# Performance work log

Hardware: AMD Instinct MI355X
Metric: run time of the kernel (lower is better)

Reference implementation:

```python
import jax, jax.numpy as jnp
import numpy as np

Z, K, H, Y = 128, 256, 512, 4  # z_size, key_size, hidden_size, y_dim


def setup_inputs() -> dict:
    key = jax.random.key(0)
    ks = jax.random.split(key, 8)
    B, T, P = 512, 32, 32
    s = lambda k, shape, sc: (jax.random.normal(k, shape, jnp.float32) * sc)
    return {
        "x_seq": jax.random.normal(ks[0], (B, T, P, P), jnp.float32),
        "W_enc": s(ks[1], (P * P, Z), 0.03),
        "gamma": jnp.ones((Z,), jnp.float32),
        "beta": jnp.zeros((Z,), jnp.float32),
        "W_ih": s(ks[2], (4 * H, K + 1), 0.05),
        "W_hh": s(ks[3], (4 * H, H), 0.04),
        "b_ih": jnp.zeros((4 * H,), jnp.float32),
        "b_hh": jnp.zeros((4 * H,), jnp.float32),
        "W_key": s(ks[4], (K, H), 0.06),
        "b_key": jnp.zeros((K,), jnp.float32),
        "W_g": s(ks[5], (1, H), 0.06),
        "b_g": jnp.zeros((1,), jnp.float32),
        "conf_gain": jnp.ones((1,), jnp.float32),
        "conf_bias": jnp.zeros((1,), jnp.float32),
        "W_y": s(ks[6], (Y, H), 0.06),
        "b_y": jnp.zeros((Y,), jnp.float32),
    }


def _lstm_cell(x, h, c, W_ih, W_hh, b_ih, b_hh):
    # PyTorch gate order: i, f, g, o
    gates = x @ W_ih.T + b_ih + h @ W_hh.T + b_hh
    i, f, g, o = jnp.split(gates, 4, axis=-1)
    c = jax.nn.sigmoid(f) * c + jax.nn.sigmoid(i) * jnp.tanh(g)
    h = jax.nn.sigmoid(o) * jnp.tanh(c)
    return h, c


def _forward(x_seq, W_enc, gamma, beta, W_ih, W_hh, b_ih, b_hh,
             W_key, b_key, W_g, b_g, conf_gain, conf_bias, W_y, b_y):
    B, T, P, _ = x_seq.shape
    # encoder: flatten -> linear to z_size (stand-in for Encoder_mlp)
    z = x_seq.reshape(B, T, P * P) @ W_enc  # [B, T, Z]
    # context norm over the sequence dim (single task segment)
    mu = z.mean(axis=1, keepdims=True)
    sig = jnp.sqrt(z.var(axis=1, keepdims=True) + 1e-8)
    z = (z - mu) / sig * gamma + beta

    M = T + 1  # T+1 steps; final step feeds a zero z_t
    z_pad = jnp.concatenate([z, jnp.zeros((B, 1, Z), z.dtype)], axis=1)  # [B, M, Z]

    h0 = jnp.zeros((B, H), z.dtype)
    c0 = jnp.zeros((B, H), z.dtype)
    kr0 = jnp.zeros((B, K + 1), z.dtype)
    Mk0 = jnp.zeros((B, M, K), z.dtype)
    Mv0 = jnp.zeros((B, M, Z), z.dtype)

    def step(carry, t):
        h, c, key_r, M_k, M_v = carry
        z_t = jax.lax.dynamic_index_in_dim(z_pad, t, axis=1, keepdims=False)  # [B, Z]
        h, c = _lstm_cell(key_r, h, c, W_ih, W_hh, b_ih, b_hh)
        key_w = jax.nn.relu(h @ W_key.T + b_key)          # [B, K]
        g = jax.nn.sigmoid(h @ W_g.T + b_g)               # [B, 1]
        y_lin = h @ W_y.T + b_y                            # [B, Y]
        # attention read over valid memory slots j < t
        scores = jnp.einsum('bz,bmz->bm', z_t, M_v)        # [B, M]
        valid = (jnp.arange(M) < t)[None, :]
        w_k = jax.nn.softmax(jnp.where(valid, scores, -1e9), axis=1)
        c_k = jax.nn.sigmoid(scores * conf_gain + conf_bias)
        kv = jnp.concatenate([M_k, c_k[..., None]], axis=2)  # [B, M, K+1]
        attn = g * jnp.einsum('bm,bmd->bd', w_k, kv)          # [B, K+1]
        key_r_new = jnp.where(t == 0, jnp.zeros_like(attn), attn)
        # append to memory at slot t
        M_k = jax.lax.dynamic_update_slice_in_dim(M_k, key_w[:, None, :], t, axis=1)
        M_v = jax.lax.dynamic_update_slice_in_dim(M_v, z_t[:, None, :], t, axis=1)
        return (h, c, key_r_new, M_k, M_v), y_lin

    _, ys = jax.lax.scan(step, (h0, c0, kr0, Mk0, Mv0), jnp.arange(M))
    return ys[-1]  # y_pred_linear from final step, [B, Y]


def reference(x_seq, W_enc, gamma, beta, W_ih, W_hh, b_ih, b_hh,
              W_key, b_key, W_g, b_g, conf_gain, conf_bias, W_y, b_y):
    y_pred_linear = _forward(x_seq, W_enc, gamma, beta, W_ih, W_hh, b_ih, b_hh,
                             W_key, b_key, W_g, b_g, conf_gain, conf_bias, W_y, b_y)
    y_pred = jnp.argmax(y_pred_linear, axis=1)
    return y_pred_linear, y_pred
```

## Files before the change

### kernel.cpp

```cpp
#include <hip/hip_runtime.h>
#include <math.h>

typedef unsigned short ushort;
typedef unsigned int uint;
typedef __bf16 bf16x8 __attribute__((ext_vector_type(8)));
typedef float f32x4 __attribute__((ext_vector_type(4)));

#define ZS    128
#define KS    256
#define HS    512
#define BATCH 512
#define TT    32
#define MM    33
#define NB    2304
#define KPAD  800
#define HOFF  272
#define LDA   800

static __device__ __forceinline__ float sigf(float x) { return 1.f / (1.f + expf(-x)); }
static __device__ __forceinline__ float bf2f(ushort u) { return __uint_as_float((uint)u << 16); }

__global__ void prep_w(const float* __restrict__ W_ih, const float* __restrict__ W_hh,
                       const float* __restrict__ W_key, const float* __restrict__ b_ih,
                       const float* __restrict__ b_hh, const float* __restrict__ b_key,
                       const float* __restrict__ W_enc,
                       ushort* __restrict__ Whi, ushort* __restrict__ Wlo,
                       ushort* __restrict__ Behi, ushort* __restrict__ Belo,
                       float* __restrict__ biasN)
{
    int idx = blockIdx.x * 256 + threadIdx.x;
    if (idx < NB) {
        float bv;
        if (idx < 2048) { int j = idx >> 2, gi = idx & 3, r = gi * 512 + j; bv = b_ih[r] + b_hh[r]; }
        else bv = b_key[idx - 2048];
        biasN[idx] = bv;
    }
    if (idx < NB * KPAD) {
        int n = idx / KPAD, k = idx - n * KPAD;
        float v = 0.f;
        if (n < 2048) {
            int j = n >> 2, gi = n & 3, r = gi * 512 + j;
            if (k < 257) v = W_ih[r * 257 + k];
            else if (k >= HOFF && k < HOFF + 512) v = W_hh[r * 512 + (k - HOFF)];
        } else {
            if (k >= HOFF && k < HOFF + 512) v = W_key[(n - 2048) * 512 + (k - HOFF)];
        }
        uint u = __float_as_uint(v);
        Whi[idx] = (ushort)(u >> 16);
        float lo = v - __uint_as_float(u & 0xFFFF0000u);
        Wlo[idx] = (ushort)(__float_as_uint(lo) >> 16);
    } else if (idx < NB * KPAD + 128 * 1024) {
        int e = idx - NB * KPAD;
        int n = e >> 10, k = e & 1023;
        float v = W_enc[k * 128 + n];
        uint u = __float_as_uint(v);
        Behi[e] = (ushort)(u >> 16);
        float lo = v - __uint_as_float(u & 0xFFFF0000u);
        Belo[e] = (ushort)(__float_as_uint(lo) >> 16);
    }
}

template<int BN, int MODE, bool PRESPLIT>
__global__ __launch_bounds__(256, 4)
void gemm_mfma(const float* __restrict__ A,
               const ushort* __restrict__ Ahi, const ushort* __restrict__ Alo, int lda,
               const ushort* __restrict__ Bhi, const ushort* __restrict__ Blo, int ldb,
               int nslice,
               float* __restrict__ out,
               ushort* __restrict__ outHi, ushort* __restrict__ outLo,
               const float* __restrict__ biasN,
               float* __restrict__ cst, float* __restrict__ Mk, int step)
{
    constexpr int NI = BN / 32;
    constexpr int AHI = 0, ALO = 32 * 40, BHI = 64 * 40, BLO = 64 * 40 + BN * 40;
    constexpr int BUF = 64 * 40 + 2 * BN * 40;
    __shared__ ushort lds[2 * BUF];

    const int tid = threadIdx.x;
    const int bx = blockIdx.x, by = blockIdx.y;
    const int row0 = by * 32, n0 = bx * BN;
    const int l = tid & 63, w = tid >> 6, wm = w >> 1, wn = w & 1;
    const int lm = l & 15, kg = (l >> 4) << 3;

    f32x4 acc[NI];
    const f32x4 zero4 = {0.f, 0.f, 0.f, 0.f};
#pragma unroll
    for (int ni = 0; ni < NI; ni++) acc[ni] = zero4;

    float4 avf;
    uint4 avu;
    uint4 bhv[BN / 64], blv[BN / 64];

    auto LOADG = [&](int s) {
        const int k0 = s * 32;
        if (PRESPLIT) {
            int idx = tid & 127, r = idx >> 2, c = (idx & 3) << 3;
            const ushort* src = (tid < 128) ? Ahi : Alo;
            avu = *(const uint4*)(src + (size_t)(row0 + r) * lda + k0 + c);
        } else {
            int r = tid >> 3, c = (tid & 7) << 2;
            avf = *(const float4*)(A + (size_t)(row0 + r) * lda + k0 + c);
        }
#pragma unroll
        for (int i = 0; i < BN / 64; i++) {
            int idx = tid + 256 * i, r = idx >> 2, c = (idx & 3) << 3;
            bhv[i] = *(const uint4*)(Bhi + (size_t)(n0 + r) * ldb + k0 + c);
            blv[i] = *(const uint4*)(Blo + (size_t)(n0 + r) * ldb + k0 + c);
        }
    };
    auto STORE = [&](int buf) {
        ushort* L = lds + buf * BUF;
        if (PRESPLIT) {
            int idx = tid & 127, r = idx >> 2, c = (idx & 3) << 3;
            *(uint4*)&L[(tid < 128 ? AHI : ALO) + r * 40 + c] = avu;
        } else {
            int r = tid >> 3, c = (tid & 7) << 2;
            uint u0 = __float_as_uint(avf.x), u1 = __float_as_uint(avf.y);
            uint u2 = __float_as_uint(avf.z), u3 = __float_as_uint(avf.w);
            uint hp0 = (u1 & 0xFFFF0000u) | (u0 >> 16);
            uint hp1 = (u3 & 0xFFFF0000u) | (u2 >> 16);
            float l0 = avf.x - __uint_as_float(u0 & 0xFFFF0000u);
            float l1 = avf.y - __uint_as_float(u1 & 0xFFFF0000u);
            float l2 = avf.z - __uint_as_float(u2 & 0xFFFF0000u);
            float l3 = avf.w - __uint_as_float(u3 & 0xFFFF0000u);
            uint lp0 = (__float_as_uint(l1) & 0xFFFF0000u) | (__float_as_uint(l0) >> 16);
            uint lp1 = (__float_as_uint(l3) & 0xFFFF0000u) | (__float_as_uint(l2) >> 16);
            *(uint2*)&L[AHI + r * 40 + c] = make_uint2(hp0, hp1);
            *(uint2*)&L[ALO + r * 40 + c] = make_uint2(lp0, lp1);
        }
#pragma unroll
        for (int i = 0; i < BN / 64; i++) {
            int idx = tid + 256 * i, r = idx >> 2, c = (idx & 3) << 3;
            *(uint4*)&L[BHI + r * 40 + c] = bhv[i];
            *(uint4*)&L[BLO + r * 40 + c] = blv[i];
        }
    };

    LOADG(0);
    STORE(0);
    for (int s = 0; s < nslice; s++) {
        if (s + 1 < nslice) LOADG(s + 1);
        __syncthreads();
        const ushort* L = lds + (s & 1) * BUF;
        bf16x8 ah, alv, bh[NI], bl[NI];
        {
            int r = wm * 16 + lm;
            ah  = *(const bf16x8*)&L[AHI + r * 40 + kg];
            alv = *(const bf16x8*)&L[ALO + r * 40 + kg];
        }
#pragma unroll
        for (int ni = 0; ni < NI; ni++) {
            int r = wn * (BN / 2) + ni * 16 + lm;
            bh[ni] = *(const bf16x8*)&L[BHI + r * 40 + kg];
            bl[ni] = *(const bf16x8*)&L[BLO + r * 40 + kg];
        }
#pragma unroll
        for (int ni = 0; ni < NI; ni++) {
            acc[ni] = __builtin_amdgcn_mfma_f32_16x16x32_bf16(ah,  bh[ni], acc[ni], 0, 0, 0);
            acc[ni] = __builtin_amdgcn_mfma_f32_16x16x32_bf16(ah,  bl[ni], acc[ni], 0, 0, 0);
            acc[ni] = __builtin_amdgcn_mfma_f32_16x16x32_bf16(alv, bh[ni], acc[ni], 0, 0, 0);
        }
        if (s + 1 < nslice) STORE((s + 1) & 1);
    }

    const int crow = (l >> 4) << 2;
    if (MODE == 0) {
#pragma unroll
        for (int ni = 0; ni < NI; ni++)
#pragma unroll
            for (int r = 0; r < 4; r++) {
                int m = row0 + wm * 16 + crow + r;
                int z = n0 + wn * (BN / 2) + ni * 16 + lm;
                out[(size_t)(m >> 5) * (MM * ZS) + (m & 31) * ZS + z] = acc[ni][r];
            }
    } else if (bx < 32) {
        __syncthreads();
        float* epi = (float*)lds;
        float* ew = epi + w * 544;
#pragma unroll
        for (int ni = 0; ni < NI; ni++)
#pragma unroll
            for (int r = 0; r < 4; r++) {
                int ml = crow + r, nl = ni * 16 + lm;
                ew[ml * 34 + nl] = acc[ni][r] + biasN[n0 + wn * 32 + nl];
            }
        __syncthreads();
        int row = tid >> 3, jj8 = tid & 7;
        int b = row0 + row;
        int j0 = bx * 16 + jj8 * 2;
        float2 cold = *(float2*)&cst[(size_t)b * HS + j0];
        float cc[2] = {cold.x, cold.y}, hv[2];
#pragma unroll
        for (int i = 0; i < 2; i++) {
            int jj = jj8 * 2 + i;
            float p[4];
#pragma unroll
            for (int g = 0; g < 4; g++) {
                int n = jj * 4 + g;
                int wv = (row >> 4) * 2 + (n >> 5);
                p[g] = epi[wv * 544 + (row & 15) * 34 + (n & 31)];
            }
            float ig = sigf(p[0]), fg = sigf(p[1]), gg = tanhf(p[2]), og = sigf(p[3]);
            float cn = fg * cc[i] + ig * gg;
            hv[i] = og * tanhf(cn);
            cc[i] = cn;
        }
        *(float2*)&cst[(size_t)b * HS + j0] = make_float2(cc[0], cc[1]);
        uint u0 = __float_as_uint(hv[0]), u1 = __float_as_uint(hv[1]);
        uint hp = (u1 & 0xFFFF0000u) | (u0 >> 16);
        float l0 = hv[0] - __uint_as_float(u0 & 0xFFFF0000u);
        float l1 = hv[1] - __uint_as_float(u1 & 0xFFFF0000u);
        uint lp = (__float_as_uint(l1) & 0xFFFF0000u) | (__float_as_uint(l0) >> 16);
        *(uint*)&outHi[(size_t)b * LDA + HOFF + j0] = hp;
        *(uint*)&outLo[(size_t)b * LDA + HOFF + j0] = lp;
    } else if (step >= 1) {
#pragma unroll
        for (int ni = 0; ni < NI; ni++)
#pragma unroll
            for (int r = 0; r < 4; r++) {
                int b = row0 + wm * 16 + crow + r;
                int cg = n0 + wn * 32 + ni * 16 + lm;
                float v = fmaxf(acc[ni][r] + biasN[cg], 0.f);
                Mk[((size_t)(step - 1) * BATCH + b) * KS + (cg - 2048)] = v;
            }
    }
}

__global__ void norm_k(float* __restrict__ z_pad, const float* __restrict__ gamma,
                       const float* __restrict__ beta)
{
    int b = blockIdx.x, zc = threadIdx.x;
    float* zb = z_pad + (size_t)b * (MM * ZS);
    float s = 0.f, s2 = 0.f;
    for (int t = 0; t < TT; t++) { float v = zb[t * ZS + zc]; s += v; s2 += v * v; }
    float mu = s * (1.f / 32.f);
    float var = s2 * (1.f / 32.f) - mu * mu;
    float rstd = 1.f / sqrtf(var + 1e-8f);
    float ga = gamma[zc], be = beta[zc];
    for (int t = 0; t < TT; t++) {
        float v = zb[t * ZS + zc];
        zb[t * ZS + zc] = (v - mu) * rstd * ga + be;
    }
    zb[TT * ZS + zc] = 0.f;
}

__global__ __launch_bounds__(256)
void scores_k(const float* __restrict__ z_pad, const float* __restrict__ cg_p,
              const float* __restrict__ cb_p, float* __restrict__ watt,
              float* __restrict__ wc)
{
    __shared__ float zs[MM * 129];
    int b = blockIdx.x, tid = threadIdx.x;
    const float* zb = z_pad + (size_t)b * (MM * ZS);
    for (int i = tid; i < MM * ZS; i += 256) {
        int m = i >> 7, k = i & 127;
        zs[m * 129 + k] = zb[i];
    }
    __syncthreads();
    float cg = cg_p[0], cb = cb_p[0];
    int wid = tid >> 6, lane = tid & 63;
    for (int t = 1 + wid; t <= 32; t += 4) {
        int m = lane;
        float s = -3.0e38f;
        if (m < t) {
            const float* zt = &zs[t * 129];
            const float* zm = &zs[m * 129];
            float acc = 0.f;
#pragma unroll 8
            for (int k = 0; k < ZS; k++) acc += zt[k] * zm[k];
            s = acc;
        }
        float mx = s;
        for (int off = 1; off < 64; off <<= 1) mx = fmaxf(mx, __shfl_xor(mx, off));
        float e = (m < t) ? expf(s - mx) : 0.f;
        float sum = e;
        for (int off = 1; off < 64; off <<= 1) sum += __shfl_xor(sum, off);
        float w = e / sum;
        if (m < t) watt[(b * MM + t) * MM + m] = w;
        float p = (m < t) ? w * sigf(s * cg + cb) : 0.f;
        for (int off = 1; off < 64; off <<= 1) p += __shfl_xor(p, off);
        if (lane == 0) wc[b * MM + t] = p;
    }
}

__global__ __launch_bounds__(256)
void post_k(ushort* __restrict__ inpHi, ushort* __restrict__ inpLo,
            const float* __restrict__ W_g, const float* __restrict__ b_g,
            const float* __restrict__ watt, const float* __restrict__ wc,
            const float* __restrict__ Mk, int t)
{
    __shared__ float red[256];
    __shared__ float wts[32];
    __shared__ float gsh;
    int b = blockIdx.x, tid = threadIdx.x;
    ushort* rHi = inpHi + (size_t)b * LDA;
    ushort* rLo = inpLo + (size_t)b * LDA;
    float h1 = bf2f(rHi[HOFF + tid]) + bf2f(rLo[HOFF + tid]);
    float h2 = bf2f(rHi[HOFF + 256 + tid]) + bf2f(rLo[HOFF + 256 + tid]);
    red[tid] = h1 * W_g[tid] + h2 * W_g[tid + 256];
    if (tid < t) wts[tid] = watt[(b * MM + t) * MM + tid];
    __syncthreads();
    for (int s = 128; s > 0; s >>= 1) {
        if (tid < s) red[tid] += red[tid + s];
        __syncthreads();
    }
    if (tid == 0) gsh = sigf(red[0] + b_g[0]);
    __syncthreads();
    float g = gsh;
    float acc = 0.f;
    for (int m = 0; m < t; m++)
        acc += wts[m] * Mk[((size_t)m * BATCH + b) * KS + tid];
    float v = g * acc;
    uint u = __float_as_uint(v);
    rHi[tid] = (ushort)(u >> 16);
    float lo = v - __uint_as_float(u & 0xFFFF0000u);
    rLo[tid] = (ushort)(__float_as_uint(lo) >> 16);
    if (tid == 0) {
        float vc = g * wc[b * MM + t];
        uint uc = __float_as_uint(vc);
        rHi[256] = (ushort)(uc >> 16);
        float lc = vc - __uint_as_float(uc & 0xFFFF0000u);
        rLo[256] = (ushort)(__float_as_uint(lc) >> 16);
    }
}

__global__ void y_k(const ushort* __restrict__ inpHi, const ushort* __restrict__ inpLo,
                    const float* __restrict__ W_y, const float* __restrict__ b_y,
                    float* __restrict__ out)
{
    int b = blockIdx.x, lane = threadIdx.x;
    const ushort* hHi = inpHi + (size_t)b * LDA + HOFF;
    const ushort* hLo = inpLo + (size_t)b * LDA + HOFF;
    float a0 = 0, a1 = 0, a2 = 0, a3 = 0;
    for (int r = 0; r < 8; r++) {
        int k = lane + r * 64;
        float hv = bf2f(hHi[k]) + bf2f(hLo[k]);
        a0 += hv * W_y[k];
        a1 += hv * W_y[512 + k];
        a2 += hv * W_y[1024 + k];
        a3 += hv * W_y[1536 + k];
    }
    for (int off = 32; off > 0; off >>= 1) {
        a0 += __shfl_xor(a0, off);
        a1 += __shfl_xor(a1, off);
        a2 += __shfl_xor(a2, off);
        a3 += __shfl_xor(a3, off);
    }
    if (lane == 0) {
        float y0 = a0 + b_y[0], y1 = a1 + b_y[1], y2 = a2 + b_y[2], y3 = a3 + b_y[3];
        out[b * 4 + 0] = y0; out[b * 4 + 1] = y1; out[b * 4 + 2] = y2; out[b * 4 + 3] = y3;
        int best = 0; float bv = y0;
        if (y1 > bv) { bv = y1; best = 1; }
        if (y2 > bv) { bv = y2; best = 2; }
        if (y3 > bv) { bv = y3; best = 3; }
        out[2048 + b] = (float)best;
    }
}

extern "C" void kernel_launch(void* const* d_in, const int* in_sizes, int n_in,
                              void* d_out, int out_size, void* d_ws, size_t ws_size,
                              hipStream_t stream)
{
    const float* x_seq = (const float*)d_in[0];
    const float* W_enc = (const float*)d_in[1];
    const float* gamma = (const float*)d_in[2];
    const float* beta  = (const float*)d_in[3];
    const float* W_ih  = (const float*)d_in[4];
    const float* W_hh  = (const float*)d_in[5];
    const float* b_ih  = (const float*)d_in[6];
    const float* b_hh  = (const float*)d_in[7];
    const float* W_key = (const float*)d_in[8];
    const float* b_key = (const float*)d_in[9];
    const float* W_g   = (const float*)d_in[10];
    const float* b_g   = (const float*)d_in[11];
    const float* cgain = (const float*)d_in[12];
    const float* cbias = (const float*)d_in[13];
    const float* W_y   = (const float*)d_in[14];
    const float* b_y   = (const float*)d_in[15];

    float* ws    = (float*)d_ws;
    float* z_pad = ws;
    float* watt  = z_pad + 2162688;
    float* wcv   = watt + 557568;
    float* Mk    = wcv + 16896;
    float* biasN = Mk + 4194304;
    float* cst   = biasN + 2304;
    ushort* inpHi0 = (ushort*)(cst + 262144);
    ushort* inpLo0 = inpHi0 + 409600;
    ushort* inpHi1 = inpLo0 + 409600;
    ushort* inpLo1 = inpHi1 + 409600;
    ushort* Whi  = inpLo1 + 409600;
    ushort* Wlo  = Whi + NB * KPAD;
    ushort* Behi = Wlo + NB * KPAD;
    ushort* Belo = Behi + 131072;

    hipMemsetAsync(cst, 0, 262144 * sizeof(float) + 4 * 409600 * sizeof(ushort), stream);

    prep_w<<<(NB * KPAD + 131072 + 255) / 256, 256, 0, stream>>>(
        W_ih, W_hh, W_key, b_ih, b_hh, b_key, W_enc, Whi, Wlo, Behi, Belo, biasN);

    gemm_mfma<128, 0, false><<<dim3(1, 512), 256, 0, stream>>>(
        x_seq, nullptr, nullptr, 1024, Behi, Belo, 1024, 32,
        z_pad, nullptr, nullptr, nullptr, nullptr, nullptr, 0);
    norm_k<<<512, 128, 0, stream>>>(z_pad, gamma, beta);
    scores_k<<<512, 256, 0, stream>>>(z_pad, cgain, cbias, watt, wcv);

    for (int t = 0; t <= 32; t++) {
        ushort* inHiC = (t & 1) ? inpHi1 : inpHi0;
        ushort* inLoC = (t & 1) ? inpLo1 : inpLo0;
        ushort* inHiN = (t & 1) ? inpHi0 : inpHi1;
        ushort* inLoN = (t & 1) ? inpLo0 : inpLo1;
        gemm_mfma<64, 1, true><<<dim3(36, 16), 256, 0, stream>>>(
            nullptr, inHiC, inLoC, LDA, Whi, Wlo, KPAD, 25,
            nullptr, inHiN, inLoN, biasN, cst, Mk, t);
        if (t >= 1 && t <= 31)
            post_k<<<512, 256, 0, stream>>>(inHiN, inLoN, W_g, b_g, watt, wcv, Mk, t);
    }
    y_k<<<512, 64, 0, stream>>>((0 ? inpHi0 : inpHi1), (0 ? inpLo0 : inpLo1),
                                W_y, b_y, (float*)d_out);
}
```

Measured before the change: 1.015 ms.

## Enlarge GEMM tiles to 64x128 and prepack weights in tile-contiguous layout

The split-bf16 MFMA GEMM moves from 32xBN tiles to 64x128 tiles, so each warp computes a 2x4 grid of MFMA outputs with more register reuse. Weights are prepacked per tile and k-slice as contiguous hi/lo blocks, which turns B loads into fully coalesced linear reads. The block index is swizzled across groups of eight. The recurrent step launch drops from 576 to 144 blocks, which cuts redundant weight traffic but lowers parallelism on a GPU with many CUs and raises register and LDS use per block.

Measured after the change: 1.758 ms. +73.3%, slower.

```diff
diff --git a/kernel.cpp b/kernel.cpp
--- a/kernel.cpp
+++ b/kernel.cpp
@@ -16,6 +16,11 @@
 #define KPAD  800
 #define HOFF  272
 #define LDA   800
+#define GTILES 18
+#define GSLICE 25
+#define ESLICE 32
+#define GP (GTILES*GSLICE*8192)
+#define EP (ESLICE*8192)
 
 static __device__ __forceinline__ float sigf(float x) { return 1.f / (1.f + expf(-x)); }
 static __device__ __forceinline__ float bf2f(ushort u) { return __uint_as_float((uint)u << 16); }
@@ -24,8 +29,7 @@
                        const float* __restrict__ W_key, const float* __restrict__ b_ih,
                        const float* __restrict__ b_hh, const float* __restrict__ b_key,
                        const float* __restrict__ W_enc,
-                       ushort* __restrict__ Whi, ushort* __restrict__ Wlo,
-                       ushort* __restrict__ Behi, ushort* __restrict__ Belo,
+                       ushort* __restrict__ Wpk, ushort* __restrict__ Epk,
                        float* __restrict__ biasN)
 {
     int idx = blockIdx.x * 256 + threadIdx.x;
@@ -35,8 +39,15 @@
         else bv = b_key[idx - 2048];
         biasN[idx] = bv;
     }
-    if (idx < NB * KPAD) {
-        int n = idx / KPAD, k = idx - n * KPAD;
+    if (idx < GP) {
+        int tile = idx / (GSLICE * 8192);
+        int rem  = idx - tile * (GSLICE * 8192);
+        int s    = rem >> 13;
+        int e2   = rem & 8191;
+        int hi_f = (e2 < 4096);
+        int e    = e2 & 4095;
+        int n = tile * 128 + (e >> 5);
+        int k = s * 32 + ((e >> 3) & 3) * 8 + (e & 7);
         float v = 0.f;
         if (n < 2048) {
             int j = n >> 2, gi = n & 3, r = gi * 512 + j;
@@ -46,183 +57,208 @@
             if (k >= HOFF && k < HOFF + 512) v = W_key[(n - 2048) * 512 + (k - HOFF)];
         }
         uint u = __float_as_uint(v);
-        Whi[idx] = (ushort)(u >> 16);
-        float lo = v - __uint_as_float(u & 0xFFFF0000u);
-        Wlo[idx] = (ushort)(__float_as_uint(lo) >> 16);
-    } else if (idx < NB * KPAD + 128 * 1024) {
-        int e = idx - NB * KPAD;
-        int n = e >> 10, k = e & 1023;
+        if (hi_f) Wpk[idx] = (ushort)(u >> 16);
+        else {
+            float lo = v - __uint_as_float(u & 0xFFFF0000u);
+            Wpk[idx] = (ushort)(__float_as_uint(lo) >> 16);
+        }
+    } else if (idx < GP + EP) {
+        int q = idx - GP;
+        int s = q >> 13;
+        int e2 = q & 8191;
+        int hi_f = (e2 < 4096);
+        int e = e2 & 4095;
+        int n = e >> 5;
+        int k = s * 32 + ((e >> 3) & 3) * 8 + (e & 7);
         float v = W_enc[k * 128 + n];
         uint u = __float_as_uint(v);
-        Behi[e] = (ushort)(u >> 16);
-        float lo = v - __uint_as_float(u & 0xFFFF0000u);
-        Belo[e] = (ushort)(__float_as_uint(lo) >> 16);
-    }
-}
-
-template<int BN, int MODE, bool PRESPLIT>
-__global__ __launch_bounds__(256, 4)
-void gemm_mfma(const float* __restrict__ A,
+        if (hi_f) Epk[idx - GP] = (ushort)(u >> 16);
+        else {
+            float lo = v - __uint_as_float(u & 0xFFFF0000u);
+            Epk[idx - GP] = (ushort)(__float_as_uint(lo) >> 16);
+        }
+    }
+}
+
+template<int MODE, bool PRESPLIT>
+__global__ __launch_bounds__(256)
+void gemm_mfma(const float* __restrict__ Af,
                const ushort* __restrict__ Ahi, const ushort* __restrict__ Alo, int lda,
-               const ushort* __restrict__ Bhi, const ushort* __restrict__ Blo, int ldb,
-               int nslice,
+               const ushort* __restrict__ Bpk, int nslice,
                float* __restrict__ out,
                ushort* __restrict__ outHi, ushort* __restrict__ outLo,
                const float* __restrict__ biasN,
                float* __restrict__ cst, float* __restrict__ Mk, int step)
 {
-    constexpr int NI = BN / 32;
-    constexpr int AHI = 0, ALO = 32 * 40, BHI = 64 * 40, BLO = 64 * 40 + BN * 40;
-    constexpr int BUF = 64 * 40 + 2 * BN * 40;
+    constexpr int AHI = 0, ALO = 2560, BHI = 5120, BLO = 10240;
+    constexpr int BUF = 15360;
     __shared__ ushort lds[2 * BUF];
 
     const int tid = threadIdx.x;
-    const int bx = blockIdx.x, by = blockIdx.y;
-    const int row0 = by * 32, n0 = bx * BN;
+    int bx, by;
+    if (MODE == 0) { bx = 0; by = blockIdx.x; }
+    else {
+        int f = blockIdx.x, xc = f & 7, ii = f >> 3;
+        int g = xc * GTILES + ii;
+        bx = g >> 3; by = g & 7;
+    }
+    const int row0 = by * 64, n0 = bx * 128;
     const int l = tid & 63, w = tid >> 6, wm = w >> 1, wn = w & 1;
     const int lm = l & 15, kg = (l >> 4) << 3;
 
-    f32x4 acc[NI];
+    f32x4 acc[2][4];
     const f32x4 zero4 = {0.f, 0.f, 0.f, 0.f};
 #pragma unroll
-    for (int ni = 0; ni < NI; ni++) acc[ni] = zero4;
-
-    float4 avf;
-    uint4 avu;
-    uint4 bhv[BN / 64], blv[BN / 64];
+    for (int mi = 0; mi < 2; mi++)
+#pragma unroll
+        for (int ni = 0; ni < 4; ni++) acc[mi][ni] = zero4;
+
+    float4 avf[2];
+    uint4 aHu, aLu;
+    uint4 bv[4];
 
     auto LOADG = [&](int s) {
         const int k0 = s * 32;
         if (PRESPLIT) {
-            int idx = tid & 127, r = idx >> 2, c = (idx & 3) << 3;
-            const ushort* src = (tid < 128) ? Ahi : Alo;
-            avu = *(const uint4*)(src + (size_t)(row0 + r) * lda + k0 + c);
+            int r = tid >> 2, c = (tid & 3) << 3;
+            aHu = *(const uint4*)(Ahi + (size_t)(row0 + r) * lda + k0 + c);
+            aLu = *(const uint4*)(Alo + (size_t)(row0 + r) * lda + k0 + c);
         } else {
-            int r = tid >> 3, c = (tid & 7) << 2;
-            avf = *(const float4*)(A + (size_t)(row0 + r) * lda + k0 + c);
-        }
-#pragma unroll
-        for (int i = 0; i < BN / 64; i++) {
-            int idx = tid + 256 * i, r = idx >> 2, c = (idx & 3) << 3;
-            bhv[i] = *(const uint4*)(Bhi + (size_t)(n0 + r) * ldb + k0 + c);
-            blv[i] = *(const uint4*)(Blo + (size_t)(n0 + r) * ldb + k0 + c);
-        }
+#pragma unroll
+            for (int i = 0; i < 2; i++) {
+                int idx = tid + 256 * i, r = idx >> 3, c = (idx & 7) << 2;
+                avf[i] = *(const float4*)(Af + (size_t)(row0 + r) * lda + k0 + c);
+            }
+        }
+        const ushort* bp = Bpk + ((size_t)bx * nslice + s) * 8192;
+#pragma unroll
+        for (int q = 0; q < 4; q++)
+            bv[q] = *(const uint4*)(bp + q * 2048 + tid * 8);
     };
     auto STORE = [&](int buf) {
         ushort* L = lds + buf * BUF;
         if (PRESPLIT) {
-            int idx = tid & 127, r = idx >> 2, c = (idx & 3) << 3;
-            *(uint4*)&L[(tid < 128 ? AHI : ALO) + r * 40 + c] = avu;
+            int r = tid >> 2, c = (tid & 3) << 3;
+            *(uint4*)&L[AHI + r * 40 + c] = aHu;
+            *(uint4*)&L[ALO + r * 40 + c] = aLu;
         } else {
-            int r = tid >> 3, c = (tid & 7) << 2;
-            uint u0 = __float_as_uint(avf.x), u1 = __float_as_uint(avf.y);
-            uint u2 = __float_as_uint(avf.z), u3 = __float_as_uint(avf.w);
-            uint hp0 = (u1 & 0xFFFF0000u) | (u0 >> 16);
-            uint hp1 = (u3 & 0xFFFF0000u) | (u2 >> 16);
-            float l0 = avf.x - __uint_as_float(u0 & 0xFFFF0000u);
-            float l1 = avf.y - __uint_as_float(u1 & 0xFFFF0000u);
-            float l2 = avf.z - __uint_as_float(u2 & 0xFFFF0000u);
-            float l3 = avf.w - __uint_as_float(u3 & 0xFFFF0000u);
-            uint lp0 = (__float_as_uint(l1) & 0xFFFF0000u) | (__float_as_uint(l0) >> 16);
-            uint lp1 = (__float_as_uint(l3) & 0xFFFF0000u) | (__float_as_uint(l2) >> 16);
-            *(uint2*)&L[AHI + r * 40 + c] = make_uint2(hp0, hp1);
-            *(uint2*)&L[ALO + r * 40 + c] = make_uint2(lp0, lp1);
-        }
-#pragma unroll
-        for (int i = 0; i < BN / 64; i++) {
-            int idx = tid + 256 * i, r = idx >> 2, c = (idx & 3) << 3;
-            *(uint4*)&L[BHI + r * 40 + c] = bhv[i];
-            *(uint4*)&L[BLO + r * 40 + c] = blv[i];
+#pragma unroll
+            for (int i = 0; i < 2; i++) {
+                int idx = tid + 256 * i, r = idx >> 3, c = (idx & 7) << 2;
+                uint u0 = __float_as_uint(avf[i].x), u1 = __float_as_uint(avf[i].y);
+                uint u2 = __float_as_uint(avf[i].z), u3 = __float_as_uint(avf[i].w);
+                uint hp0 = (u1 & 0xFFFF0000u) | (u0 >> 16);
+                uint hp1 = (u3 & 0xFFFF0000u) | (u2 >> 16);
+                float l0 = avf[i].x - __uint_as_float(u0 & 0xFFFF0000u);
+                float l1 = avf[i].y - __uint_as_float(u1 & 0xFFFF0000u);
+                float l2 = avf[i].z - __uint_as_float(u2 & 0xFFFF0000u);
+                float l3 = avf[i].w - __uint_as_float(u3 & 0xFFFF0000u);
+                uint lp0 = (__float_as_uint(l1) & 0xFFFF0000u) | (__float_as_uint(l0) >> 16);
+                uint lp1 = (__float_as_uint(l3) & 0xFFFF0000u) | (__float_as_uint(l2) >> 16);
+                *(uint2*)&L[AHI + r * 40 + c] = make_uint2(hp0, hp1);
+                *(uint2*)&L[ALO + r * 40 + c] = make_uint2(lp0, lp1);
+            }
+        }
+#pragma unroll
+        for (int q = 0; q < 2; q++) {
+            int idx = tid + 256 * q, r = idx >> 2, c = (idx & 3) << 3;
+            *(uint4*)&L[BHI + r * 40 + c] = bv[q];
+            *(uint4*)&L[BLO + r * 40 + c] = bv[2 + q];
         }
     };
 
     LOADG(0);
     STORE(0);
     for (int s = 0; s < nslice; s++) {
+        __syncthreads();
         if (s + 1 < nslice) LOADG(s + 1);
-        __syncthreads();
         const ushort* L = lds + (s & 1) * BUF;
-        bf16x8 ah, alv, bh[NI], bl[NI];
-        {
-            int r = wm * 16 + lm;
-            ah  = *(const bf16x8*)&L[AHI + r * 40 + kg];
-            alv = *(const bf16x8*)&L[ALO + r * 40 + kg];
-        }
-#pragma unroll
-        for (int ni = 0; ni < NI; ni++) {
-            int r = wn * (BN / 2) + ni * 16 + lm;
-            bh[ni] = *(const bf16x8*)&L[BHI + r * 40 + kg];
-            bl[ni] = *(const bf16x8*)&L[BLO + r * 40 + kg];
-        }
-#pragma unroll
-        for (int ni = 0; ni < NI; ni++) {
-            acc[ni] = __builtin_amdgcn_mfma_f32_16x16x32_bf16(ah,  bh[ni], acc[ni], 0, 0, 0);
-            acc[ni] = __builtin_amdgcn_mfma_f32_16x16x32_bf16(ah,  bl[ni], acc[ni], 0, 0, 0);
-            acc[ni] = __builtin_amdgcn_mfma_f32_16x16x32_bf16(alv, bh[ni], acc[ni], 0, 0, 0);
-        }
+        bf16x8 ah[2], al2[2], bh[4], bl2[4];
+#pragma unroll
+        for (int mi = 0; mi < 2; mi++) {
+            int r = wm * 32 + mi * 16 + lm;
+            ah[mi]  = *(const bf16x8*)&L[AHI + r * 40 + kg];
+            al2[mi] = *(const bf16x8*)&L[ALO + r * 40 + kg];
+        }
+#pragma unroll
+        for (int ni = 0; ni < 4; ni++) {
+            int r = wn * 64 + ni * 16 + lm;
+            bh[ni]  = *(const bf16x8*)&L[BHI + r * 40 + kg];
+            bl2[ni] = *(const bf16x8*)&L[BLO + r * 40 + kg];
+        }
+#pragma unroll
+        for (int mi = 0; mi < 2; mi++)
+#pragma unroll
+            for (int ni = 0; ni < 4; ni++) {
+                acc[mi][ni] = __builtin_amdgcn_mfma_f32_16x16x32_bf16(ah[mi],  bh[ni],  acc[mi][ni], 0, 0, 0);
+                acc[mi][ni] = __builtin_amdgcn_mfma_f32_16x16x32_bf16(ah[mi],  bl2[ni], acc[mi][ni], 0, 0, 0);
+                acc[mi][ni] = __builtin_amdgcn_mfma_f32_16x16x32_bf16(al2[mi], bh[ni],  acc[mi][ni], 0, 0, 0);
+            }
         if (s + 1 < nslice) STORE((s + 1) & 1);
     }
 
     const int crow = (l >> 4) << 2;
     if (MODE == 0) {
 #pragma unroll
-        for (int ni = 0; ni < NI; ni++)
-#pragma unroll
-            for (int r = 0; r < 4; r++) {
-                int m = row0 + wm * 16 + crow + r;
-                int z = n0 + wn * (BN / 2) + ni * 16 + lm;
-                out[(size_t)(m >> 5) * (MM * ZS) + (m & 31) * ZS + z] = acc[ni][r];
-            }
-    } else if (bx < 32) {
+        for (int mi = 0; mi < 2; mi++)
+#pragma unroll
+            for (int ni = 0; ni < 4; ni++)
+#pragma unroll
+                for (int r_ = 0; r_ < 4; r_++) {
+                    int m = row0 + wm * 32 + mi * 16 + crow + r_;
+                    int z = wn * 64 + ni * 16 + lm;
+                    out[(size_t)(m >> 5) * (MM * ZS) + (m & 31) * ZS + z] = acc[mi][ni][r_];
+                }
+    } else if (bx < 16) {
         __syncthreads();
         float* epi = (float*)lds;
-        float* ew = epi + w * 544;
-#pragma unroll
-        for (int ni = 0; ni < NI; ni++)
-#pragma unroll
-            for (int r = 0; r < 4; r++) {
-                int ml = crow + r, nl = ni * 16 + lm;
-                ew[ml * 34 + nl] = acc[ni][r] + biasN[n0 + wn * 32 + nl];
-            }
+#pragma unroll
+        for (int mi = 0; mi < 2; mi++)
+#pragma unroll
+            for (int ni = 0; ni < 4; ni++)
+#pragma unroll
+                for (int r_ = 0; r_ < 4; r_++) {
+                    int ml = wm * 32 + mi * 16 + crow + r_;
+                    int nl = wn * 64 + ni * 16 + lm;
+                    epi[ml * 132 + nl] = acc[mi][ni][r_] + biasN[n0 + nl];
+                }
         __syncthreads();
-        int row = tid >> 3, jj8 = tid & 7;
-        int b = row0 + row;
-        int j0 = bx * 16 + jj8 * 2;
-        float2 cold = *(float2*)&cst[(size_t)b * HS + j0];
-        float cc[2] = {cold.x, cold.y}, hv[2];
-#pragma unroll
-        for (int i = 0; i < 2; i++) {
-            int jj = jj8 * 2 + i;
-            float p[4];
-#pragma unroll
-            for (int g = 0; g < 4; g++) {
-                int n = jj * 4 + g;
-                int wv = (row >> 4) * 2 + (n >> 5);
-                p[g] = epi[wv * 544 + (row & 15) * 34 + (n & 31)];
-            }
-            float ig = sigf(p[0]), fg = sigf(p[1]), gg = tanhf(p[2]), og = sigf(p[3]);
-            float cn = fg * cc[i] + ig * gg;
-            hv[i] = og * tanhf(cn);
-            cc[i] = cn;
-        }
-        *(float2*)&cst[(size_t)b * HS + j0] = make_float2(cc[0], cc[1]);
-        uint u0 = __float_as_uint(hv[0]), u1 = __float_as_uint(hv[1]);
-        uint hp = (u1 & 0xFFFF0000u) | (u0 >> 16);
-        float l0 = hv[0] - __uint_as_float(u0 & 0xFFFF0000u);
-        float l1 = hv[1] - __uint_as_float(u1 & 0xFFFF0000u);
-        uint lp = (__float_as_uint(l1) & 0xFFFF0000u) | (__float_as_uint(l0) >> 16);
-        *(uint*)&outHi[(size_t)b * LDA + HOFF + j0] = hp;
-        *(uint*)&outLo[(size_t)b * LDA + HOFF + j0] = lp;
+        int bl_ = tid & 63, jj4 = tid >> 6;
+        int b = row0 + bl_;
+        int j0 = bx * 32 + jj4 * 8;
+        float4 c0 = *(float4*)&cst[(size_t)b * HS + j0];
+        float4 c1 = *(float4*)&cst[(size_t)b * HS + j0 + 4];
+        float cc[8] = {c0.x, c0.y, c0.z, c0.w, c1.x, c1.y, c1.z, c1.w};
+        ushort h_hi[8] __attribute__((aligned(16)));
+        ushort h_lo[8] __attribute__((aligned(16)));
+#pragma unroll
+        for (int u = 0; u < 8; u++) {
+            const float* pr = &epi[bl_ * 132 + jj4 * 32 + u * 4];
+            float ig = sigf(pr[0]), fg = sigf(pr[1]), gg = tanhf(pr[2]), og = sigf(pr[3]);
+            float cn = fg * cc[u] + ig * gg;
+            float hv = og * tanhf(cn);
+            cc[u] = cn;
+            uint uu = __float_as_uint(hv);
+            h_hi[u] = (ushort)(uu >> 16);
+            float lo = hv - __uint_as_float(uu & 0xFFFF0000u);
+            h_lo[u] = (ushort)(__float_as_uint(lo) >> 16);
+        }
+        *(float4*)&cst[(size_t)b * HS + j0]     = make_float4(cc[0], cc[1], cc[2], cc[3]);
+        *(float4*)&cst[(size_t)b * HS + j0 + 4] = make_float4(cc[4], cc[5], cc[6], cc[7]);
+        *(uint4*)&outHi[(size_t)b * LDA + HOFF + j0] = *(uint4*)h_hi;
+        *(uint4*)&outLo[(size_t)b * LDA + HOFF + j0] = *(uint4*)h_lo;
     } else if (step >= 1) {
 #pragma unroll
-        for (int ni = 0; ni < NI; ni++)
-#pragma unroll
-            for (int r = 0; r < 4; r++) {
-                int b = row0 + wm * 16 + crow + r;
-                int cg = n0 + wn * 32 + ni * 16 + lm;
-                float v = fmaxf(acc[ni][r] + biasN[cg], 0.f);
-                Mk[((size_t)(step - 1) * BATCH + b) * KS + (cg - 2048)] = v;
-            }
+        for (int mi = 0; mi < 2; mi++)
+#pragma unroll
+            for (int ni = 0; ni < 4; ni++)
+#pragma unroll
+                for (int r_ = 0; r_ < 4; r_++) {
+                    int b = row0 + wm * 32 + mi * 16 + crow + r_;
+                    int nl = wn * 64 + ni * 16 + lm;
+                    float v = fmaxf(acc[mi][ni][r_] + biasN[n0 + nl], 0.f);
+                    Mk[((size_t)(step - 1) * BATCH + b) * KS + (n0 - 2048 + nl)] = v;
+                }
     }
 }
 
@@ -389,18 +425,16 @@
     ushort* inpLo0 = inpHi0 + 409600;
     ushort* inpHi1 = inpLo0 + 409600;
     ushort* inpLo1 = inpHi1 + 409600;
-    ushort* Whi  = inpLo1 + 409600;
-    ushort* Wlo  = Whi + NB * KPAD;
-    ushort* Behi = Wlo + NB * KPAD;
-    ushort* Belo = Behi + 131072;
+    ushort* Wpk  = inpLo1 + 409600;
+    ushort* Epk  = Wpk + GP;
 
     hipMemsetAsync(cst, 0, 262144 * sizeof(float) + 4 * 409600 * sizeof(ushort), stream);
 
-    prep_w<<<(NB * KPAD + 131072 + 255) / 256, 256, 0, stream>>>(
-        W_ih, W_hh, W_key, b_ih, b_hh, b_key, W_enc, Whi, Wlo, Behi, Belo, biasN);
-
-    gemm_mfma<128, 0, false><<<dim3(1, 512), 256, 0, stream>>>(
-        x_seq, nullptr, nullptr, 1024, Behi, Belo, 1024, 32,
+    prep_w<<<(GP + EP + 255) / 256, 256, 0, stream>>>(
+        W_ih, W_hh, W_key, b_ih, b_hh, b_key, W_enc, Wpk, Epk, biasN);
+
+    gemm_mfma<0, false><<<256, 256, 0, stream>>>(
+        x_seq, nullptr, nullptr, 1024, Epk, ESLICE,
         z_pad, nullptr, nullptr, nullptr, nullptr, nullptr, 0);
     norm_k<<<512, 128, 0, stream>>>(z_pad, gamma, beta);
     scores_k<<<512, 256, 0, stream>>>(z_pad, cgain, cbias, watt, wcv);
@@ -410,12 +444,11 @@
         ushort* inLoC = (t & 1) ? inpLo1 : inpLo0;
         ushort* inHiN = (t & 1) ? inpHi0 : inpHi1;
         ushort* inLoN = (t & 1) ? inpLo0 : inpLo1;
-        gemm_mfma<64, 1, true><<<dim3(36, 16), 256, 0, stream>>>(
-            nullptr, inHiC, inLoC, LDA, Whi, Wlo, KPAD, 25,
+        gemm_mfma<1, true><<<GTILES * 8, 256, 0, stream>>>(
+            nullptr, inHiC, inLoC, LDA, Wpk, GSLICE,
             nullptr, inHiN, inLoN, biasN, cst, Mk, t);
         if (t >= 1 && t <= 31)
             post_k<<<512, 256, 0, stream>>>(inHiN, inLoN, W_g, b_g, watt, wcv, Mk, t);
     }
-    y_k<<<512, 64, 0, stream>>>((0 ? inpHi0 : inpHi1), (0 ? inpLo0 : inpLo1),
-                                W_y, b_y, (float*)d_out);
-}
+    y_k<<<512, 64, 0, stream>>>(inpHi1, inpLo1, W_y, b_y, (float*)d_out);
+}
```
